# Kernel tuning notes

Measured on AMD Instinct MI355X. Metric: run time of the kernel, lower is better.

## Reference

```python
import jax, jax.numpy as jnp
import numpy as np

TABLE_SIZE = 256
I16_MIN, I16_MAX = -32768.0, 32767.0
I8_MIN, I8_MAX = -128.0, 127.0
MAX_SOFTMAX_VALUE = 1.0
OUT_SCALE = MAX_SOFTMAX_VALUE * 2.0 / 255.0            # int8 output scale
EXP_OUT_SCALE = 2.0 / 65535.0                          # qint16 exp output scale
RECIP_OUT_SCALE = (1.0 / 0.1) * 2.0 / 65535.0          # qint16 reciprocal output scale
# (xmin, xmax, kind) in ascending x order; 'table' = 256-entry LUT, 'line' = linear fit
EXP_REGIONS = [(-40.0, -20.0, 'line'), (-20.0, -10.0, 'table'), (-10.0, 0.0, 'table'), (0.0, 1.0, 'line')]
RECIP_REGIONS = [(0.001, 0.1, 'line'), (0.1, 250.0, 'table'), (250.0, 500.0, 'table'), (500.0, 700.0, 'line')]


def _quant(y, out_scale, qmin, qmax):
    return jnp.clip(jnp.round(y / out_scale), qmin, qmax)


def _piecewise(x, func, regions, out_scale, qmin, qmax):
    """Piecewise quantized approximation of func: constant / line / 256-entry
    table regions, returning quantized (integer-valued float) outputs."""
    left_c = _quant(func(jnp.float32(regions[0][0])), out_scale, qmin, qmax)
    y = left_c * jnp.ones_like(x)
    for xmin, xmax, kind in regions:
        if kind == 'table':
            xs = jnp.linspace(xmin, xmax, TABLE_SIZE)
            tab = _quant(func(xs), out_scale, qmin, qmax)
            idx = jnp.clip(jnp.round((x - xmin) * ((TABLE_SIZE - 1) / (xmax - xmin))), 0, TABLE_SIZE - 1).astype(jnp.int32)
            y_r = tab[idx]
        else:
            y0 = func(jnp.float32(xmin))
            y1 = func(jnp.float32(xmax))
            y_r = _quant(y0 + (x - xmin) * ((y1 - y0) / (xmax - xmin)), out_scale, qmin, qmax)
        y = jnp.where(x >= xmin, y_r, y)
    right_c = _quant(func(jnp.float32(regions[-1][1])), out_scale, qmin, qmax)
    return jnp.where(x > regions[-1][1], right_c, y)


def setup_inputs() -> dict:
    key = jax.random.key(0)
    k1, _ = jax.random.split(key)
    data = jax.random.randint(k1, (32, 128, 80, 80), -128, 128, dtype=jnp.int32)  # int8 repr, zp=0
    data_scale = jnp.array([0.0625], dtype=jnp.float32)
    return {"data": data, "data_scale": data_scale}


def reference(data, data_scale):
    ds = data_scale[0]
    C = data.shape[1]
    shift = float(np.ceil(np.log2(C)))  # rescale_shift for the exp-sum
    # max-subtract in the integer domain, dequantize diff (zero_point = 0)
    qmax = jnp.max(data, axis=1, keepdims=True)
    xd = (data - qmax).astype(jnp.float32) * ds  # [B,C,H,W], in (-inf, 0]
    # quantized exp via piecewise tables -> qint16 with EXP_OUT_SCALE
    exp_q = _piecewise(xd, jnp.exp, EXP_REGIONS, EXP_OUT_SCALE, I16_MIN, I16_MAX)
    # sum over channels, right-shift back into int16 range
    sum_q = jnp.sum(exp_q, axis=1, keepdims=True)
    sum_sh = jnp.clip(jnp.round(sum_q * (2.0 ** -shift)), I16_MIN, I16_MAX)
    div_scale = EXP_OUT_SCALE * (2.0 ** shift)  # div_data_scale
    # quantized reciprocal of the (dequantized) shifted sum -> qint16
    recip_q = _piecewise(sum_sh * div_scale, lambda v: 1.0 / v, RECIP_REGIONS, RECIP_OUT_SCALE, I16_MIN, I16_MAX)
    # out = exp * recip, requantized to int8 with OUT_SCALE, then dequantized
    out_q = jnp.clip(jnp.round(exp_q * recip_q * (EXP_OUT_SCALE * RECIP_OUT_SCALE / OUT_SCALE)), I8_MIN, I8_MAX)
    return out_q * OUT_SCALE
```

## Files before the change

kernel.cpp:

```cpp
#include <hip/hip_runtime.h>
#include <cmath>

#define NB  32
#define NC  128
#define NHW 6400
#define PIX 64
#define TPB 256

typedef float vfloat4 __attribute__((ext_vector_type(4)));


__global__ __launch_bounds__(TPB) void qsoftmax_kernel(
    const int* __restrict__ data,
    const float* __restrict__ dscale,
    float* __restrict__ out) {
#pragma clang fp contract(off)
  __shared__ int   exp_tab[256];
  __shared__ float recip_tab[256];
  __shared__ int4  red_m[16][16];
  __shared__ int4  red_s[16][16];

  const int t  = threadIdx.x;
  const int k  = t >> 4;
  const int p4 = t & 15;

  const int blk  = blockIdx.x;
  const int b    = blk / (NHW / PIX);
  const int hw0  = (blk % (NHW / PIX)) * PIX;
  const int base4 = b * NC * (NHW / 4) + (hw0 >> 2);

  const float ds = dscale[0];

  {
    const float EXP_SCALE_F = (float)(2.0 / 65535.0);
    float x = (float)(-t) * ds;
    float e;
    if (x >= 0.0f) {
      float y0 = expf(0.0f), y1 = expf(1.0f);
      e = rintf((y0 + x * ((y1 - y0) / 1.0f)) / EXP_SCALE_F);
    } else if (x >= -10.0f) {
      float delta = 10.0f / 255.0f;
      float idxf = rintf((x + 10.0f) * 25.5f);
      idxf = fminf(fmaxf(idxf, 0.0f), 255.0f);
      float xs = -10.0f + idxf * delta;
      e = rintf((float)exp((double)xs) / EXP_SCALE_F);
    } else {
      float delta = 10.0f / 255.0f;
      float idxf = rintf((x + 20.0f) * 25.5f);
      idxf = fminf(fmaxf(idxf, 0.0f), 255.0f);
      float xs = -20.0f + idxf * delta;
      e = rintf((float)exp((double)xs) / EXP_SCALE_F);
    }
    e = fminf(fmaxf(e, -32768.0f), 32767.0f);
    exp_tab[t] = (int)e;

    const float RECIP_SCALE_F = (float)((1.0 / 0.1) * 2.0 / 65535.0);
    float deltar = (250.0f - 0.1f) / 255.0f;
    float xs = 0.1f + (float)t * deltar;
    float r = rintf((1.0f / xs) / RECIP_SCALE_F);
    r = fminf(fmaxf(r, -32768.0f), 32767.0f);
    recip_tab[t] = r;
  }

  const int4* g4 = (const int4*)data;
  int pd[8];
  int4 m = make_int4(-128, -128, -128, -128);
#pragma unroll
  for (int i = 0; i < 8; ++i) {
    int4 v = g4[base4 + (16 * i + k) * (NHW / 4) + p4];
    m.x = max(m.x, v.x); m.y = max(m.y, v.y);
    m.z = max(m.z, v.z); m.w = max(m.w, v.w);
    pd[i] = (v.x & 255) | ((v.y & 255) << 8) | ((v.z & 255) << 16) |
            (int)((unsigned)(v.w & 255) << 24);
  }
  red_m[k][p4] = m;
  __syncthreads();

  int4 q = red_m[0][p4];
#pragma unroll
  for (int kk = 1; kk < 16; ++kk) {
    int4 r = red_m[kk][p4];
    q.x = max(q.x, r.x); q.y = max(q.y, r.y);
    q.z = max(q.z, r.z); q.w = max(q.w, r.w);
  }

  int pe[16];
  int4 s = make_int4(0, 0, 0, 0);
#pragma unroll
  for (int i = 0; i < 8; ++i) {
    int pdv = pd[i];
    int c0 = (pdv << 24) >> 24;
    int c1 = (pdv << 16) >> 24;
    int c2 = (pdv << 8) >> 24;
    int c3 = pdv >> 24;
    int e0 = exp_tab[q.x - c0];
    int e1 = exp_tab[q.y - c1];
    int e2 = exp_tab[q.z - c2];
    int e3 = exp_tab[q.w - c3];
    s.x += e0; s.y += e1; s.z += e2; s.w += e3;
    pe[2 * i]     = e0 | (e1 << 16);
    pe[2 * i + 1] = e2 | (e3 << 16);
  }
  red_s[k][p4] = s;
  __syncthreads();

  int4 tot = red_s[0][p4];
#pragma unroll
  for (int kk = 1; kk < 16; ++kk) {
    int4 r = red_s[kk][p4];
    tot.x += r.x; tot.y += r.y; tot.z += r.z; tot.w += r.w;
  }
  const float DIV_SCALE_F = (float)((2.0 / 65535.0) * 128.0);
  const float RIDX_K_F    = (float)(255.0 / (250.0 - 0.1));
  float rq[4];
  {
    int tv[4] = {tot.x, tot.y, tot.z, tot.w};
#pragma unroll
    for (int j = 0; j < 4; ++j) {
      float ss = rintf((float)tv[j] * 0.0078125f);
      ss = fminf(fmaxf(ss, -32768.0f), 32767.0f);
      float v = ss * DIV_SCALE_F;
      float idxf = rintf((v - 0.1f) * RIDX_K_F);
      idxf = fminf(fmaxf(idxf, 0.0f), 255.0f);
      rq[j] = recip_tab[(int)idxf];
    }
  }

  const float K_F = (float)((2.0 / 65535.0) * ((1.0 / 0.1) * 2.0 / 65535.0) / (2.0 / 255.0));
  const float OUT_SCALE_F = (float)(2.0 / 255.0);
  vfloat4* o4 = (vfloat4*)out;
#pragma unroll
  for (int i = 0; i < 8; ++i) {
    int pa = pe[2 * i], pb = pe[2 * i + 1];
    float e0 = (float)(pa & 0xFFFF);
    float e1 = (float)(pa >> 16);
    float e2 = (float)(pb & 0xFFFF);
    float e3 = (float)(pb >> 16);
    vfloat4 o;
    o.x = fminf(fmaxf(rintf((e0 * rq[0]) * K_F), -128.0f), 127.0f) * OUT_SCALE_F;
    o.y = fminf(fmaxf(rintf((e1 * rq[1]) * K_F), -128.0f), 127.0f) * OUT_SCALE_F;
    o.z = fminf(fmaxf(rintf((e2 * rq[2]) * K_F), -128.0f), 127.0f) * OUT_SCALE_F;
    o.w = fminf(fmaxf(rintf((e3 * rq[3]) * K_F), -128.0f), 127.0f) * OUT_SCALE_F;
    o4[base4 + (16 * i + k) * (NHW / 4) + p4] = o;
  }
}

extern "C" void kernel_launch(void* const* d_in, const int* in_sizes, int n_in,
                              void* d_out, int out_size, void* d_ws, size_t ws_size,
                              hipStream_t stream) {
  const int* data     = (const int*)d_in[0];
  const float* dscale = (const float*)d_in[1];
  float* out          = (float*)d_out;
  (void)in_sizes; (void)n_in; (void)d_ws; (void)ws_size; (void)out_size;

  dim3 grid(NB * (NHW / PIX));
  qsoftmax_kernel<<<grid, TPB, 0, stream>>>(data, dscale, out);
}
```

Before: 189.5 us.

## Process two pixel tiles per block with all loads issued before LUT build

Each block now covers 128 pixels as two 64-pixel tiles. All 16 global int4 loads for both tiles are issued up front, before the exp/recip lookup tables are built, so memory latency overlaps table construction. The table-build cost is amortised over twice the data. Other changes: double-buffered reduction arrays, a custom LDS barrier that waits only on lgkmcnt, nontemporal output stores, and launch_bounds with min 4 blocks. In exchange the grid is halved and register pressure rises (16 int4 held live), which may reduce occupancy.

```diff
diff --git a/kernel.cpp b/kernel.cpp
--- a/kernel.cpp
+++ b/kernel.cpp
@@ -4,32 +4,121 @@
 #define NB  32
 #define NC  128
 #define NHW 6400
-#define PIX 64
 #define TPB 256
 
 typedef float vfloat4 __attribute__((ext_vector_type(4)));
 
+#define LDS_BARRIER()                                        \
+  do {                                                       \
+    asm volatile("s_waitcnt lgkmcnt(0)" ::: "memory");       \
+    __builtin_amdgcn_s_barrier();                            \
+    asm volatile("" ::: "memory");                           \
+  } while (0)
 
-__global__ __launch_bounds__(TPB) void qsoftmax_kernel(
+#define PROCESS_TILE(PAR, V, BASE4T)                                           \
+  do {                                                                         \
+    int pd[8];                                                                 \
+    int4 m = make_int4(-128, -128, -128, -128);                                \
+    _Pragma("unroll")                                                          \
+    for (int i = 0; i < 8; ++i) {                                              \
+      int4 v = (V)[i];                                                         \
+      m.x = max(m.x, v.x); m.y = max(m.y, v.y);                                \
+      m.z = max(m.z, v.z); m.w = max(m.w, v.w);                                \
+      pd[i] = (v.x & 255) | ((v.y & 255) << 8) | ((v.z & 255) << 16) |         \
+              (int)((unsigned)(v.w & 255) << 24);                              \
+    }                                                                          \
+    red_m[PAR][k][p4] = m;                                                     \
+    LDS_BARRIER();                                                             \
+    int4 q = red_m[PAR][0][p4];                                                \
+    _Pragma("unroll")                                                          \
+    for (int kk = 1; kk < 16; ++kk) {                                          \
+      int4 r = red_m[PAR][kk][p4];                                             \
+      q.x = max(q.x, r.x); q.y = max(q.y, r.y);                                \
+      q.z = max(q.z, r.z); q.w = max(q.w, r.w);                                \
+    }                                                                          \
+    int pe[16];                                                                \
+    int4 s = make_int4(0, 0, 0, 0);                                            \
+    _Pragma("unroll")                                                          \
+    for (int i = 0; i < 8; ++i) {                                              \
+      int pdv = pd[i];                                                         \
+      int c0 = (pdv << 24) >> 24;                                              \
+      int c1 = (pdv << 16) >> 24;                                              \
+      int c2 = (pdv << 8) >> 24;                                               \
+      int c3 = pdv >> 24;                                                      \
+      int e0 = exp_tab[q.x - c0];                 \
+      int e1 = exp_tab[q.y - c1];                                              \
+      int e2 = exp_tab[q.z - c2];                                              \
+      int e3 = exp_tab[q.w - c3];                                              \
+      s.x += e0; s.y += e1; s.z += e2; s.w += e3;                              \
+      pe[2 * i]     = e0 | (e1 << 16);                                         \
+      pe[2 * i + 1] = e2 | (e3 << 16);                                         \
+    }                                                                          \
+    red_s[PAR][k][p4] = s;                                                     \
+    LDS_BARRIER();                                                             \
+    int4 tot = red_s[PAR][0][p4];                                              \
+    _Pragma("unroll")                                                          \
+    for (int kk = 1; kk < 16; ++kk) {                                          \
+      int4 r = red_s[PAR][kk][p4];                                             \
+      tot.x += r.x; tot.y += r.y; tot.z += r.z; tot.w += r.w;                  \
+    }                                                                          \
+    float rq[4];                                                               \
+    {                                                                          \
+      int tv[4] = {tot.x, tot.y, tot.z, tot.w};                                \
+      _Pragma("unroll")                                                        \
+      for (int j = 0; j < 4; ++j) {                                            \
+        float ss = rintf((float)tv[j] * 0.0078125f);                           \
+        ss = fminf(fmaxf(ss, -32768.0f), 32767.0f);                            \
+        float vv = ss * DIV_SCALE_F;                                           \
+        float idxf = rintf((vv - 0.1f) * RIDX_K_F);                            \
+        idxf = fminf(fmaxf(idxf, 0.0f), 255.0f);                               \
+        rq[j] = recip_tab[(int)idxf];                                          \
+      }                                                                        \
+    }                                                                          \
+    _Pragma("unroll")                                                          \
+    for (int i = 0; i < 8; ++i) {                                              \
+      int pa = pe[2 * i], pb = pe[2 * i + 1];                                  \
+      float e0 = (float)(pa & 0xFFFF);                                         \
+      float e1 = (float)(pa >> 16);                                            \
+      float e2 = (float)(pb & 0xFFFF);                                         \
+      float e3 = (float)(pb >> 16);                                            \
+      vfloat4 o;                                                               \
+      o.x = fminf(fmaxf(rintf((e0 * rq[0]) * K_F), -128.0f), 127.0f) * OUT_SCALE_F; \
+      o.y = fminf(fmaxf(rintf((e1 * rq[1]) * K_F), -128.0f), 127.0f) * OUT_SCALE_F; \
+      o.z = fminf(fmaxf(rintf((e2 * rq[2]) * K_F), -128.0f), 127.0f) * OUT_SCALE_F; \
+      o.w = fminf(fmaxf(rintf((e3 * rq[3]) * K_F), -128.0f), 127.0f) * OUT_SCALE_F; \
+      __builtin_nontemporal_store(o, &o4[(BASE4T) + (16 * i + k) * (NHW / 4) + p4]); \
+    }                                                                          \
+  } while (0)
+
+__global__ __launch_bounds__(TPB, 4) void qsoftmax_kernel(
     const int* __restrict__ data,
     const float* __restrict__ dscale,
     float* __restrict__ out) {
 #pragma clang fp contract(off)
   __shared__ int   exp_tab[256];
   __shared__ float recip_tab[256];
-  __shared__ int4  red_m[16][16];
-  __shared__ int4  red_s[16][16];
+  __shared__ int4  red_m[2][16][16];
+  __shared__ int4  red_s[2][16][16];
 
   const int t  = threadIdx.x;
   const int k  = t >> 4;
   const int p4 = t & 15;
 
   const int blk  = blockIdx.x;
-  const int b    = blk / (NHW / PIX);
-  const int hw0  = (blk % (NHW / PIX)) * PIX;
+  const int b    = blk / (NHW / 128);
+  const int hw0  = (blk % (NHW / 128)) * 128;
   const int base4 = b * NC * (NHW / 4) + (hw0 >> 2);
 
   const float ds = dscale[0];
+
+  const int4* g4 = (const int4*)data;
+  int4 vA[8], vB[8];
+#pragma unroll
+  for (int i = 0; i < 8; ++i)
+    vA[i] = g4[base4 + (16 * i + k) * (NHW / 4) + p4];
+#pragma unroll
+  for (int i = 0; i < 8; ++i)
+    vB[i] = g4[base4 + 16 + (16 * i + k) * (NHW / 4) + p4];
 
   {
     const float EXP_SCALE_F = (float)(2.0 / 65535.0);
@@ -61,88 +150,16 @@
     r = fminf(fmaxf(r, -32768.0f), 32767.0f);
     recip_tab[t] = r;
   }
+  LDS_BARRIER();
 
-  const int4* g4 = (const int4*)data;
-  int pd[8];
-  int4 m = make_int4(-128, -128, -128, -128);
-#pragma unroll
-  for (int i = 0; i < 8; ++i) {
-    int4 v = g4[base4 + (16 * i + k) * (NHW / 4) + p4];
-    m.x = max(m.x, v.x); m.y = max(m.y, v.y);
-    m.z = max(m.z, v.z); m.w = max(m.w, v.w);
-    pd[i] = (v.x & 255) | ((v.y & 255) << 8) | ((v.z & 255) << 16) |
-            (int)((unsigned)(v.w & 255) << 24);
-  }
-  red_m[k][p4] = m;
-  __syncthreads();
+  const float DIV_SCALE_F  = (float)((2.0 / 65535.0) * 128.0);
+  const float RIDX_K_F     = (float)(255.0 / (250.0 - 0.1));
+  const float K_F          = (float)((2.0 / 65535.0) * ((1.0 / 0.1) * 2.0 / 65535.0) / (2.0 / 255.0));
+  const float OUT_SCALE_F  = (float)(2.0 / 255.0);
+  vfloat4* o4 = (vfloat4*)out;
 
-  int4 q = red_m[0][p4];
-#pragma unroll
-  for (int kk = 1; kk < 16; ++kk) {
-    int4 r = red_m[kk][p4];
-    q.x = max(q.x, r.x); q.y = max(q.y, r.y);
-    q.z = max(q.z, r.z); q.w = max(q.w, r.w);
-  }
-
-  int pe[16];
-  int4 s = make_int4(0, 0, 0, 0);
-#pragma unroll
-  for (int i = 0; i < 8; ++i) {
-    int pdv = pd[i];
-    int c0 = (pdv << 24) >> 24;
-    int c1 = (pdv << 16) >> 24;
-    int c2 = (pdv << 8) >> 24;
-    int c3 = pdv >> 24;
-    int e0 = exp_tab[q.x - c0];
-    int e1 = exp_tab[q.y - c1];
-    int e2 = exp_tab[q.z - c2];
-    int e3 = exp_tab[q.w - c3];
-    s.x += e0; s.y += e1; s.z += e2; s.w += e3;
-    pe[2 * i]     = e0 | (e1 << 16);
-    pe[2 * i + 1] = e2 | (e3 << 16);
-  }
-  red_s[k][p4] = s;
-  __syncthreads();
-
-  int4 tot = red_s[0][p4];
-#pragma unroll
-  for (int kk = 1; kk < 16; ++kk) {
-    int4 r = red_s[kk][p4];
-    tot.x += r.x; tot.y += r.y; tot.z += r.z; tot.w += r.w;
-  }
-  const float DIV_SCALE_F = (float)((2.0 / 65535.0) * 128.0);
-  const float RIDX_K_F    = (float)(255.0 / (250.0 - 0.1));
-  float rq[4];
-  {
-    int tv[4] = {tot.x, tot.y, tot.z, tot.w};
-#pragma unroll
-    for (int j = 0; j < 4; ++j) {
-      float ss = rintf((float)tv[j] * 0.0078125f);
-      ss = fminf(fmaxf(ss, -32768.0f), 32767.0f);
-      float v = ss * DIV_SCALE_F;
-      float idxf = rintf((v - 0.1f) * RIDX_K_F);
-      idxf = fminf(fmaxf(idxf, 0.0f), 255.0f);
-      rq[j] = recip_tab[(int)idxf];
-    }
-  }
-
-  const float K_F = (float)((2.0 / 65535.0) * ((1.0 / 0.1) * 2.0 / 65535.0) / (2.0 / 255.0));
-  const float OUT_SCALE_F = (float)(2.0 / 255.0);
-  vfloat4* o4 = (vfloat4*)out;
-#pragma unroll
-  for (int i = 0; i < 8; ++i) {
-    int pa = pe[2 * i], pb = pe[2 * i + 1];
-    float e0 = (float)(pa & 0xFFFF);
-    float e1 = (float)(pa >> 16);
-    float e2 = (float)(pb & 0xFFFF);
-    float e3 = (float)(pb >> 16);
-    vfloat4 o;
-    o.x = fminf(fmaxf(rintf((e0 * rq[0]) * K_F), -128.0f), 127.0f) * OUT_SCALE_F;
-    o.y = fminf(fmaxf(rintf((e1 * rq[1]) * K_F), -128.0f), 127.0f) * OUT_SCALE_F;
-    o.z = fminf(fmaxf(rintf((e2 * rq[2]) * K_F), -128.0f), 127.0f) * OUT_SCALE_F;
-    o.w = fminf(fmaxf(rintf((e3 * rq[3]) * K_F), -128.0f), 127.0f) * OUT_SCALE_F;
-    o4[base4 + (16 * i + k) * (NHW / 4) + p4] = o;
-  }
+  PROCESS_TILE(0, vA, base4);
+  PROCESS_TILE(1, vB, base4 + 16);
 }
 
 extern "C" void kernel_launch(void* const* d_in, const int* in_sizes, int n_in,
@@ -153,6 +170,6 @@
   float* out          = (float*)d_out;
   (void)in_sizes; (void)n_in; (void)d_ws; (void)ws_size; (void)out_size;
 
-  dim3 grid(NB * (NHW / PIX));
+  dim3 grid(NB * (NHW / 128));
   qsoftmax_kernel<<<grid, TPB, 0, stream>>>(data, dscale, out);
 }
```

After: 186.6 us. Within noise of the previous version (-1.5%).

## Split softmax into stats and expand kernels with workspace; nontemporal stores

Applied to the files above, without the earlier changes.

Splits the fused single-pass kernel into a stats kernel and a grid-stride expand kernel. The stats kernel computes per-pixel channel max and reciprocal and writes them to workspace. The expand kernel re-reads the input and writes outputs with nontemporal stores, and the monolithic kernel stays as a fallback when no workspace is available. This re-reads the 52MB input, adds a second launch and may be slower. It appears aimed at streaming write efficiency and lower register pressure.

```diff
diff --git a/kernel.cpp b/kernel.cpp
--- a/kernel.cpp
+++ b/kernel.cpp
@@ -6,11 +6,197 @@
 #define NHW 6400
 #define PIX 64
 #define TPB 256
+#define NQ4 (NHW / 4)
+#define NQUAD (NB * NQ4)
 
 typedef float vfloat4 __attribute__((ext_vector_type(4)));
 
-
-__global__ __launch_bounds__(TPB) void qsoftmax_kernel(
+__global__ __launch_bounds__(TPB) void qsoftmax_stats_kernel(
+    const int* __restrict__ data,
+    const float* __restrict__ dscale,
+    int* __restrict__ qp_ws,
+    float4* __restrict__ rec_ws) {
+#pragma clang fp contract(off)
+  __shared__ int   exp_tab[256];
+  __shared__ float recip_tab[256];
+  __shared__ int4  red_m[16][16];
+  __shared__ int4  red_s[16][16];
+
+  const int t  = threadIdx.x;
+  const int k  = t >> 4;
+  const int p4 = t & 15;
+
+  const int blk  = blockIdx.x;
+  const int b    = blk / (NHW / PIX);
+  const int hw0  = (blk % (NHW / PIX)) * PIX;
+  const int base4 = b * NC * NQ4 + (hw0 >> 2);
+
+  const float ds = dscale[0];
+
+  {
+    const float EXP_SCALE_F = (float)(2.0 / 65535.0);
+    float x = (float)(-t) * ds;
+    float e;
+    if (x >= 0.0f) {
+      float y0 = expf(0.0f), y1 = expf(1.0f);
+      e = rintf((y0 + x * ((y1 - y0) / 1.0f)) / EXP_SCALE_F);
+    } else if (x >= -10.0f) {
+      float delta = 10.0f / 255.0f;
+      float idxf = rintf((x + 10.0f) * 25.5f);
+      idxf = fminf(fmaxf(idxf, 0.0f), 255.0f);
+      float xs = -10.0f + idxf * delta;
+      e = rintf((float)exp((double)xs) / EXP_SCALE_F);
+    } else {
+      float delta = 10.0f / 255.0f;
+      float idxf = rintf((x + 20.0f) * 25.5f);
+      idxf = fminf(fmaxf(idxf, 0.0f), 255.0f);
+      float xs = -20.0f + idxf * delta;
+      e = rintf((float)exp((double)xs) / EXP_SCALE_F);
+    }
+    e = fminf(fmaxf(e, -32768.0f), 32767.0f);
+    exp_tab[t] = (int)e;
+
+    const float RECIP_SCALE_F = (float)((1.0 / 0.1) * 2.0 / 65535.0);
+    float deltar = (250.0f - 0.1f) / 255.0f;
+    float xs = 0.1f + (float)t * deltar;
+    float r = rintf((1.0f / xs) / RECIP_SCALE_F);
+    r = fminf(fmaxf(r, -32768.0f), 32767.0f);
+    recip_tab[t] = r;
+  }
+
+  const int4* g4 = (const int4*)data;
+  int pd[8];
+  int4 m = make_int4(-128, -128, -128, -128);
+#pragma unroll
+  for (int i = 0; i < 8; ++i) {
+    int4 v = g4[base4 + (16 * i + k) * NQ4 + p4];
+    m.x = max(m.x, v.x); m.y = max(m.y, v.y);
+    m.z = max(m.z, v.z); m.w = max(m.w, v.w);
+    pd[i] = (v.x & 255) | ((v.y & 255) << 8) | ((v.z & 255) << 16) |
+            (int)((unsigned)(v.w & 255) << 24);
+  }
+  red_m[k][p4] = m;
+  __syncthreads();
+
+  int4 q = red_m[0][p4];
+#pragma unroll
+  for (int kk = 1; kk < 16; ++kk) {
+    int4 r = red_m[kk][p4];
+    q.x = max(q.x, r.x); q.y = max(q.y, r.y);
+    q.z = max(q.z, r.z); q.w = max(q.w, r.w);
+  }
+
+  int4 s = make_int4(0, 0, 0, 0);
+#pragma unroll
+  for (int i = 0; i < 8; ++i) {
+    int pdv = pd[i];
+    int c0 = (pdv << 24) >> 24;
+    int c1 = (pdv << 16) >> 24;
+    int c2 = (pdv << 8) >> 24;
+    int c3 = pdv >> 24;
+    s.x += exp_tab[q.x - c0];
+    s.y += exp_tab[q.y - c1];
+    s.z += exp_tab[q.z - c2];
+    s.w += exp_tab[q.w - c3];
+  }
+  red_s[k][p4] = s;
+  __syncthreads();
+
+  int4 tot = red_s[0][p4];
+#pragma unroll
+  for (int kk = 1; kk < 16; ++kk) {
+    int4 r = red_s[kk][p4];
+    tot.x += r.x; tot.y += r.y; tot.z += r.z; tot.w += r.w;
+  }
+  const float DIV_SCALE_F = (float)((2.0 / 65535.0) * 128.0);
+  const float RIDX_K_F    = (float)(255.0 / (250.0 - 0.1));
+  float rq[4];
+  {
+    int tv[4] = {tot.x, tot.y, tot.z, tot.w};
+#pragma unroll
+    for (int j = 0; j < 4; ++j) {
+      float ss = rintf((float)tv[j] * 0.0078125f);
+      ss = fminf(fmaxf(ss, -32768.0f), 32767.0f);
+      float v = ss * DIV_SCALE_F;
+      float idxf = rintf((v - 0.1f) * RIDX_K_F);
+      idxf = fminf(fmaxf(idxf, 0.0f), 255.0f);
+      rq[j] = recip_tab[(int)idxf];
+    }
+  }
+
+  if (k == 0) {
+    const int sq = b * NQ4 + (hw0 >> 2) + p4;
+    qp_ws[sq] = (q.x & 255) | ((q.y & 255) << 8) | ((q.z & 255) << 16) |
+                (int)((unsigned)(q.w & 255) << 24);
+    rec_ws[sq] = make_float4(rq[0], rq[1], rq[2], rq[3]);
+  }
+}
+
+__global__ __launch_bounds__(TPB) void qsoftmax_expand_kernel(
+    const int* __restrict__ data,
+    const float* __restrict__ dscale,
+    const int* __restrict__ qp_ws,
+    const float4* __restrict__ rec_ws,
+    float* __restrict__ out) {
+#pragma clang fp contract(off)
+  __shared__ int exp_tab[256];
+
+  const int t = threadIdx.x;
+  const float ds = dscale[0];
+
+  {
+    const float EXP_SCALE_F = (float)(2.0 / 65535.0);
+    float x = (float)(-t) * ds;
+    float e;
+    if (x >= 0.0f) {
+      float y0 = expf(0.0f), y1 = expf(1.0f);
+      e = rintf((y0 + x * ((y1 - y0) / 1.0f)) / EXP_SCALE_F);
+    } else if (x >= -10.0f) {
+      float delta = 10.0f / 255.0f;
+      float idxf = rintf((x + 10.0f) * 25.5f);
+      idxf = fminf(fmaxf(idxf, 0.0f), 255.0f);
+      float xs = -10.0f + idxf * delta;
+      e = rintf((float)exp((double)xs) / EXP_SCALE_F);
+    } else {
+      float delta = 10.0f / 255.0f;
+      float idxf = rintf((x + 20.0f) * 25.5f);
+      idxf = fminf(fmaxf(idxf, 0.0f), 255.0f);
+      float xs = -20.0f + idxf * delta;
+      e = rintf((float)exp((double)xs) / EXP_SCALE_F);
+    }
+    e = fminf(fmaxf(e, -32768.0f), 32767.0f);
+    exp_tab[t] = (int)e;
+  }
+  __syncthreads();
+
+  const float K_F = (float)((2.0 / 65535.0) * ((1.0 / 0.1) * 2.0 / 65535.0) / (2.0 / 255.0));
+  const float OUT_SCALE_F = (float)(2.0 / 255.0);
+
+  const int total4 = NB * NC * NQ4;
+  const int4* g4 = (const int4*)data;
+  vfloat4* o4 = (vfloat4*)out;
+
+  for (int u = blockIdx.x * TPB + t; u < total4; u += gridDim.x * TPB) {
+    int4 v = g4[u];
+    const int quad = u % NQ4;
+    const int b    = u / (NQ4 * NC);
+    const int pq   = b * NQ4 + quad;
+    const int qp   = qp_ws[pq];
+    const float4 rv = rec_ws[pq];
+    float e0 = (float)exp_tab[((qp << 24) >> 24) - v.x];
+    float e1 = (float)exp_tab[((qp << 16) >> 24) - v.y];
+    float e2 = (float)exp_tab[((qp << 8) >> 24) - v.z];
+    float e3 = (float)exp_tab[(qp >> 24) - v.w];
+    vfloat4 o;
+    o.x = fminf(fmaxf(rintf((e0 * rv.x) * K_F), -128.0f), 127.0f) * OUT_SCALE_F;
+    o.y = fminf(fmaxf(rintf((e1 * rv.y) * K_F), -128.0f), 127.0f) * OUT_SCALE_F;
+    o.z = fminf(fmaxf(rintf((e2 * rv.z) * K_F), -128.0f), 127.0f) * OUT_SCALE_F;
+    o.w = fminf(fmaxf(rintf((e3 * rv.w) * K_F), -128.0f), 127.0f) * OUT_SCALE_F;
+    __builtin_nontemporal_store(o, &o4[u]);
+  }
+}
+
+__global__ __launch_bounds__(TPB) void qsoftmax_mono_kernel(
     const int* __restrict__ data,
     const float* __restrict__ dscale,
     float* __restrict__ out) {
@@ -27,7 +213,7 @@
   const int blk  = blockIdx.x;
   const int b    = blk / (NHW / PIX);
   const int hw0  = (blk % (NHW / PIX)) * PIX;
-  const int base4 = b * NC * (NHW / 4) + (hw0 >> 2);
+  const int base4 = b * NC * NQ4 + (hw0 >> 2);
 
   const float ds = dscale[0];
 
@@ -67,7 +253,7 @@
   int4 m = make_int4(-128, -128, -128, -128);
 #pragma unroll
   for (int i = 0; i < 8; ++i) {
-    int4 v = g4[base4 + (16 * i + k) * (NHW / 4) + p4];
+    int4 v = g4[base4 + (16 * i + k) * NQ4 + p4];
     m.x = max(m.x, v.x); m.y = max(m.y, v.y);
     m.z = max(m.z, v.z); m.w = max(m.w, v.w);
     pd[i] = (v.x & 255) | ((v.y & 255) << 8) | ((v.z & 255) << 16) |
@@ -141,7 +327,7 @@
     o.y = fminf(fmaxf(rintf((e1 * rq[1]) * K_F), -128.0f), 127.0f) * OUT_SCALE_F;
     o.z = fminf(fmaxf(rintf((e2 * rq[2]) * K_F), -128.0f), 127.0f) * OUT_SCALE_F;
     o.w = fminf(fmaxf(rintf((e3 * rq[3]) * K_F), -128.0f), 127.0f) * OUT_SCALE_F;
-    o4[base4 + (16 * i + k) * (NHW / 4) + p4] = o;
+    __builtin_nontemporal_store(o, &o4[base4 + (16 * i + k) * NQ4 + p4]);
   }
 }
 
@@ -151,8 +337,18 @@
   const int* data     = (const int*)d_in[0];
   const float* dscale = (const float*)d_in[1];
   float* out          = (float*)d_out;
-  (void)in_sizes; (void)n_in; (void)d_ws; (void)ws_size; (void)out_size;
-
-  dim3 grid(NB * (NHW / PIX));
-  qsoftmax_kernel<<<grid, TPB, 0, stream>>>(data, dscale, out);
+  (void)in_sizes; (void)n_in; (void)out_size;
+
+  const size_t need = (size_t)NQUAD * 4 + (size_t)NQUAD * 16;
+  if (d_ws != nullptr && ws_size >= need) {
+    int*    qp_ws  = (int*)d_ws;
+    float4* rec_ws = (float4*)((char*)d_ws + (size_t)NQUAD * 4);
+    qsoftmax_stats_kernel<<<dim3(NB * (NHW / PIX)), dim3(TPB), 0, stream>>>(
+        data, dscale, qp_ws, rec_ws);
+    qsoftmax_expand_kernel<<<dim3(2048), dim3(TPB), 0, stream>>>(
+        data, dscale, qp_ws, rec_ws, out);
+  } else {
+    qsoftmax_mono_kernel<<<dim3(NB * (NHW / PIX)), dim3(TPB), 0, stream>>>(
+        data, dscale, out);
+  }
 }
```

New measurement: 200.4 us. 5.8% more time.
